# Kernel tuning notes

Hardware: AMD Instinct MI355X
Metric: run time of the kernel (lower is better)

The kernel has to match this reference:

```python
import jax, jax.numpy as jnp
import numpy as np

B, IN_DIM, OUT_DIM, MV = 8192, 256, 256, 8


def setup_inputs() -> dict:
    key = jax.random.key(0)
    k1, k2 = jax.random.split(key)
    x = jax.random.normal(k1, (B, IN_DIM, MV), dtype=jnp.float32)
    weights = jax.random.normal(k2, (IN_DIM, OUT_DIM, MV), dtype=jnp.float32) * 0.01
    bias = jnp.zeros((OUT_DIM, MV), dtype=jnp.float32)
    return {"x": x, "weights": weights, "bias": bias}


def reference(x, weights, bias):
    # Simplified GA-3D geometric product, summed over in_dim (j), per out_dim (i):
    #   y[..., i, 0] = sum_j x[..., j, 0]*W[j,i,0] + x[..., j, 1]*W[j,i,1] + x[..., j, 2]*W[j,i,2]
    #   y[..., i, 4] = sum_j x[..., j, 1]*W[j,i,2] - x[..., j, 2]*W[j,i,1] + x[..., j, 4]*W[j,i,0]
    #   all other multivector components receive only the bias.
    # Scalar component: dot over first 3 multivector slots.
    c0 = jnp.einsum('bjk,jik->bi', x[..., 0:3], weights[..., 0:3])  # (B, OUT_DIM)
    # Bivector component e23: x1*w2 - x2*w1 + x4*w0.
    xv = jnp.stack([x[..., 1], -x[..., 2], x[..., 4]], axis=-1)          # (B, IN_DIM, 3)
    wv = jnp.stack([weights[..., 2], weights[..., 1], weights[..., 0]], axis=-1)  # (IN_DIM, OUT_DIM, 3)
    c4 = jnp.einsum('bjk,jik->bi', xv, wv)  # (B, OUT_DIM)
    y = jnp.broadcast_to(bias, (x.shape[0],) + bias.shape)  # (B, OUT_DIM, MV)
    y = y.at[..., 0].add(c0).at[..., 4].add(c4)
    return y
```

## Files before the change

### kernel.cpp

```cpp
#include <hip/hip_runtime.h>
#include <hip/hip_bf16.h>

typedef __attribute__((ext_vector_type(4))) float f32x4;
typedef __attribute__((ext_vector_type(8))) short bf16x8;
typedef __attribute__((ext_vector_type(4))) short short4v;

#define AROW 264
#define CS 516

__device__ __forceinline__ short f2bf(float f) {
  __hip_bfloat16 h = __float2bfloat16(f);
  return __builtin_bit_cast(short, h);
}

__global__ __launch_bounds__(256) void ga_prep_B(const float* __restrict__ W,
                                                 short* __restrict__ Bp) {
  const int gid = blockIdx.x * 256 + threadIdx.x;
  const int l  = gid & 63;
  const int cg = (gid >> 6) & 31;
  const int it = gid >> 11;
  const int ln = l & 15, q = l >> 4;
  const int hc = cg >> 4;
  const int i  = (cg & 15) * 16 + ln;
  const int j0 = it * 8 + q * 2;
  const float4* W4 = (const float4*)W;

  bf16x8 o;
#pragma unroll
  for (int jj = 0; jj < 2; ++jj) {
    const float4 wv = W4[((j0 + jj) * 256 + i) * 2];
    if (!hc) {
      o[jj * 4 + 0] = f2bf(wv.x); o[jj * 4 + 1] = f2bf(wv.y);
      o[jj * 4 + 2] = f2bf(wv.z); o[jj * 4 + 3] = 0;
    } else {
      o[jj * 4 + 0] = 0;           o[jj * 4 + 1] = f2bf(wv.z);
      o[jj * 4 + 2] = f2bf(-wv.y); o[jj * 4 + 3] = f2bf(wv.x);
    }
  }
  *(bf16x8*)&Bp[(size_t)gid * 8] = o;
}

__global__ __launch_bounds__(512, 2) void ga_mv_main(
    const float* __restrict__ x, const short* __restrict__ Bp,
    const float* __restrict__ bias, float* __restrict__ y) {
  __shared__ __align__(16) char smem[33088];
  short* Abuf[2] = {(short*)smem, (short*)(smem + 16 * AROW * 2)};
  float* c_lds = (float*)smem;

  const int t = threadIdx.x;
  const int bm = blockIdx.x;
  const int lane = t & 63, w = t >> 6;
  const int ln = lane & 15, qq = lane >> 4;
  const int R0 = bm * 16;

  const int ci = t & 127, rb = t >> 7;
  const int jl = ci >> 1, h2 = ci & 1;
  const float4* x4 = (const float4*)x;
  float4 fr[4];

#define LOADX(qtr)                                                           \
  {                                                                          \
    _Pragma("unroll")                                                        \
    for (int i = 0; i < 4; ++i)                                              \
      fr[i] = x4[(size_t)(R0 + rb + 4 * i) * 512 + (qtr) * 128 + ci];        \
  }

#define PROC(dst)                                                            \
  {                                                                          \
    _Pragma("unroll")                                                        \
    for (int i = 0; i < 4; ++i) {                                            \
      const float c4 = __shfl_xor(fr[i].x, 1, 64);                           \
      if (!h2) {                                                             \
        short4v a;                                                           \
        a[0] = f2bf(fr[i].x); a[1] = f2bf(fr[i].y);                          \
        a[2] = f2bf(fr[i].z); a[3] = f2bf(c4);                               \
        *(short4v*)&(dst)[(rb + 4 * i) * AROW + jl * 4] = a;                 \
      }                                                                      \
    }                                                                        \
  }

  const size_t bbase = (size_t)w * 4 * 512 + lane * 8;
  bf16x8 Bf[2][4];
#define LB(itv, b)                                                           \
  {                                                                          \
    const short* p = Bp + (size_t)(itv) * 32 * 512 + bbase;                  \
    Bf[b][0] = *(const bf16x8*)(p);                                          \
    Bf[b][1] = *(const bf16x8*)(p + 512);                                    \
    Bf[b][2] = *(const bf16x8*)(p + 1024);                                   \
    Bf[b][3] = *(const bf16x8*)(p + 1536);                                   \
  }

  LOADX(0);
  PROC(Abuf[0]);
  __syncthreads();
  LB(0, 0);
  LB(1, 1);
  LOADX(1);

  f32x4 acc[4] = {};

#pragma unroll
  for (int q = 0; q < 4; ++q) {
    const short* Ac = Abuf[q & 1];
#pragma unroll
    for (int tau = 0; tau < 8; ++tau) {
      const int it = q * 8 + tau;
      if (tau == 4 && q < 3) {
        PROC(Abuf[(q + 1) & 1]);
        if (q < 2) LOADX(q + 2);
      }
      const bf16x8 af = *(const bf16x8*)&Ac[ln * AROW + (tau * 8 + qq * 2) * 4];
#pragma unroll
      for (int n = 0; n < 4; ++n)
        acc[n] = __builtin_amdgcn_mfma_f32_16x16x32_bf16(af, Bf[it & 1][n],
                                                         acc[n], 0, 0, 0);
      if (it + 2 < 32) LB(it + 2, it & 1);
    }
    __syncthreads();
  }

#pragma unroll
  for (int n = 0; n < 4; ++n)
#pragma unroll
    for (int r = 0; r < 4; ++r)
      c_lds[(qq * 4 + r) * CS + w * 64 + n * 16 + ln] = acc[n][r];
  __syncthreads();

  const int h = t & 1, p = t >> 1;
  const float4 bv = ((const float4*)bias)[p * 2 + h];
  float4* y4 = (float4*)y;
#pragma unroll
  for (int r = 0; r < 16; ++r) {
    float4 o = bv;
    o.x += c_lds[r * CS + h * 256 + p];
    y4[((size_t)(R0 + r) * 256 + p) * 2 + h] = o;
  }
}

extern "C" void kernel_launch(void* const* d_in, const int* in_sizes, int n_in,
                              void* d_out, int out_size, void* d_ws, size_t ws_size,
                              hipStream_t stream) {
  const float* x = (const float*)d_in[0];
  const float* W = (const float*)d_in[1];
  const float* bias = (const float*)d_in[2];
  float* y = (float*)d_out;
  short* Bp = (short*)d_ws;

  ga_prep_B<<<dim3(256), dim3(256), 0, stream>>>(W, Bp);
  ga_mv_main<<<dim3(512), dim3(512), 0, stream>>>(x, Bp, bias, y);
}
```

Baseline: 132.6 us.

## Double rows per block with 1024-thread blocks and deeper B prefetch

Each block now handles 32 rows with 1024 threads. Each wave computes a 32x32 output tile (two A fragments times two B fragments) instead of 16x64, so every B fragment loaded from global memory feeds two MFMAs. The B-register prefetch ring grows from two stages to four. The epilogue is split into two LDS passes with nontemporal output stores. The grid is halved to 256 blocks, which lowers occupancy headroom and may leave some CUs underused.

After: 128.7 us. -2.9%, faster.

```diff
diff --git a/kernel.cpp b/kernel.cpp
--- a/kernel.cpp
+++ b/kernel.cpp
@@ -40,18 +40,18 @@
   *(bf16x8*)&Bp[(size_t)gid * 8] = o;
 }
 
-__global__ __launch_bounds__(512, 2) void ga_mv_main(
+__global__ __launch_bounds__(1024, 4) void ga_mv_main(
     const float* __restrict__ x, const short* __restrict__ Bp,
     const float* __restrict__ bias, float* __restrict__ y) {
-  __shared__ __align__(16) char smem[33088];
-  short* Abuf[2] = {(short*)smem, (short*)(smem + 16 * AROW * 2)};
+  __shared__ __align__(16) char smem[33792];
+  short* Abuf[2] = {(short*)smem, (short*)(smem + 32 * AROW * 2)};
   float* c_lds = (float*)smem;
 
   const int t = threadIdx.x;
   const int bm = blockIdx.x;
   const int lane = t & 63, w = t >> 6;
   const int ln = lane & 15, qq = lane >> 4;
-  const int R0 = bm * 16;
+  const int R0 = bm * 32;
 
   const int ci = t & 127, rb = t >> 7;
   const int jl = ci >> 1, h2 = ci & 1;
@@ -62,7 +62,7 @@
   {                                                                          \
     _Pragma("unroll")                                                        \
     for (int i = 0; i < 4; ++i)                                              \
-      fr[i] = x4[(size_t)(R0 + rb + 4 * i) * 512 + (qtr) * 128 + ci];        \
+      fr[i] = x4[(size_t)(R0 + rb + 8 * i) * 512 + (qtr) * 128 + ci];        \
   }
 
 #define PROC(dst)                                                            \
@@ -74,20 +74,18 @@
         short4v a;                                                           \
         a[0] = f2bf(fr[i].x); a[1] = f2bf(fr[i].y);                          \
         a[2] = f2bf(fr[i].z); a[3] = f2bf(c4);                               \
-        *(short4v*)&(dst)[(rb + 4 * i) * AROW + jl * 4] = a;                 \
+        *(short4v*)&(dst)[(rb + 8 * i) * AROW + jl * 4] = a;                 \
       }                                                                      \
     }                                                                        \
   }
 
-  const size_t bbase = (size_t)w * 4 * 512 + lane * 8;
-  bf16x8 Bf[2][4];
+  const size_t bbase = (size_t)w * 1024 + lane * 8;
+  bf16x8 Bf[4][2];
 #define LB(itv, b)                                                           \
   {                                                                          \
-    const short* p = Bp + (size_t)(itv) * 32 * 512 + bbase;                  \
+    const short* p = Bp + (size_t)(itv) * 16384 + bbase;                     \
     Bf[b][0] = *(const bf16x8*)(p);                                          \
     Bf[b][1] = *(const bf16x8*)(p + 512);                                    \
-    Bf[b][2] = *(const bf16x8*)(p + 1024);                                   \
-    Bf[b][3] = *(const bf16x8*)(p + 1536);                                   \
   }
 
   LOADX(0);
@@ -95,9 +93,11 @@
   __syncthreads();
   LB(0, 0);
   LB(1, 1);
+  LB(2, 2);
+  LB(3, 3);
   LOADX(1);
 
-  f32x4 acc[4] = {};
+  f32x4 acc[2][2] = {};
 
 #pragma unroll
   for (int q = 0; q < 4; ++q) {
@@ -109,31 +109,42 @@
         PROC(Abuf[(q + 1) & 1]);
         if (q < 2) LOADX(q + 2);
       }
-      const bf16x8 af = *(const bf16x8*)&Ac[ln * AROW + (tau * 8 + qq * 2) * 4];
+      const bf16x8 af0 = *(const bf16x8*)&Ac[ln * AROW + (tau * 8 + qq * 2) * 4];
+      const bf16x8 af1 = *(const bf16x8*)&Ac[(16 + ln) * AROW + (tau * 8 + qq * 2) * 4];
 #pragma unroll
-      for (int n = 0; n < 4; ++n)
-        acc[n] = __builtin_amdgcn_mfma_f32_16x16x32_bf16(af, Bf[it & 1][n],
-                                                         acc[n], 0, 0, 0);
-      if (it + 2 < 32) LB(it + 2, it & 1);
+      for (int n = 0; n < 2; ++n) {
+        acc[0][n] = __builtin_amdgcn_mfma_f32_16x16x32_bf16(af0, Bf[it & 3][n],
+                                                            acc[0][n], 0, 0, 0);
+        acc[1][n] = __builtin_amdgcn_mfma_f32_16x16x32_bf16(af1, Bf[it & 3][n],
+                                                            acc[1][n], 0, 0, 0);
+      }
+      if (it + 4 < 32) LB(it + 4, it & 3);
     }
     __syncthreads();
   }
 
+  const int h = t & 1, p = (t >> 1) & 255, rh = t >> 9;
+  const float4 bv = ((const float4*)bias)[p * 2 + h];
+  f32x4* y4 = (f32x4*)y;
+
 #pragma unroll
-  for (int n = 0; n < 4; ++n)
+  for (int ep = 0; ep < 2; ++ep) {
+    if (ep) __syncthreads();
 #pragma unroll
-    for (int r = 0; r < 4; ++r)
-      c_lds[(qq * 4 + r) * CS + w * 64 + n * 16 + ln] = acc[n][r];
-  __syncthreads();
-
-  const int h = t & 1, p = t >> 1;
-  const float4 bv = ((const float4*)bias)[p * 2 + h];
-  float4* y4 = (float4*)y;
+    for (int n = 0; n < 2; ++n)
 #pragma unroll
-  for (int r = 0; r < 16; ++r) {
-    float4 o = bv;
-    o.x += c_lds[r * CS + h * 256 + p];
-    y4[((size_t)(R0 + r) * 256 + p) * 2 + h] = o;
+      for (int r = 0; r < 4; ++r)
+        c_lds[(qq * 4 + r) * CS + w * 32 + n * 16 + ln] = acc[ep][n][r];
+    __syncthreads();
+#pragma unroll
+    for (int rr = 0; rr < 8; ++rr) {
+      const int row = rr * 2 + rh;
+      f32x4 o;
+      o[0] = bv.x; o[1] = bv.y; o[2] = bv.z; o[3] = bv.w;
+      o[0] += c_lds[row * CS + h * 256 + p];
+      __builtin_nontemporal_store(
+          o, &y4[((size_t)(R0 + ep * 16 + row) * 256 + p) * 2 + h]);
+    }
   }
 }
 
@@ -147,5 +158,5 @@
   short* Bp = (short*)d_ws;
 
   ga_prep_B<<<dim3(256), dim3(256), 0, stream>>>(W, Bp);
-  ga_mv_main<<<dim3(512), dim3(512), 0, stream>>>(x, Bp, bias, y);
+  ga_mv_main<<<dim3(256), dim3(1024), 0, stream>>>(x, Bp, bias, y);
 }
```
